# Kernel tuning notes

Hardware: AMD Instinct MI355X
Metric: run time of the kernel (lower is better)

The kernel has to match this reference:

```python
import jax, jax.numpy as jnp
import numpy as np

B, SEQ, NNODES = 4, 12, 1024
SEG_LEN, SEG_NUM = 3, 4
HID, FF, DK, NH, NLAYERS = 64, 2048, 32, 8, 2


def setup_inputs() -> dict:
    key = jax.random.key(0)
    ks = iter(jax.random.split(key, 64))
    def nrm(shape, scale=0.05):
        return jax.random.normal(next(ks), shape, dtype=jnp.float32) * scale
    ones = lambda s: jnp.ones(s, jnp.float32)
    zeros = lambda s: jnp.zeros(s, jnp.float32)
    S, L = 2, NLAYERS
    return {
        'traffic': nrm((B, SEQ, NNODES), 1.0),
        'user': nrm((B, SEQ, NNODES), 1.0),
        'patch_w': nrm((S, HID, SEG_LEN)), 'patch_b': nrm((S, HID)),
        'mha_w': nrm((S, L, 3 * HID, HID)), 'mha_b': nrm((S, L, 3 * HID)),
        'out_w': nrm((S, L, HID, HID)), 'out_b': nrm((S, L, HID)),
        'ff1_w': nrm((S, L, FF, HID)), 'ff1_b': nrm((S, L, FF)),
        'ff2_w': nrm((S, L, HID, FF)), 'ff2_b': nrm((S, L, HID)),
        'ln1_g': ones((S, L, HID)), 'ln1_b': zeros((S, L, HID)),
        'ln2_g': ones((S, L, HID)), 'ln2_b': zeros((S, L, HID)),
        'ga_wq': nrm((S, L, DK, HID)), 'ga_wk': nrm((S, L, DK, HID)), 'ga_wv': nrm((S, L, HID, HID)),
        'ga_ff1_w': nrm((S, L, FF, HID)), 'ga_ff1_b': nrm((S, L, FF)),
        'ga_ff2_w': nrm((S, L, HID, FF)), 'ga_ff2_b': nrm((S, L, HID)),
        'ga_ln1_g': ones((S, L, HID)), 'ga_ln1_b': zeros((S, L, HID)),
        'ga_ln2_g': ones((S, L, HID)), 'ga_ln2_b': zeros((S, L, HID)),
        'ca_wq': nrm((DK, 2 * HID)), 'ca_wk': nrm((DK, 2 * HID)), 'ca_wv': nrm((HID, 2 * HID)),
    }


def _ln(x, g, b, eps=1e-5):
    m = x.mean(-1, keepdims=True)
    v = jnp.mean((x - m) ** 2, -1, keepdims=True)
    return (x - m) / jnp.sqrt(v + eps) * g + b


def _pe(s, d):
    pos = jnp.arange(s, dtype=jnp.float32)[:, None]
    div = jnp.exp(jnp.arange(0, d, 2, dtype=jnp.float32) * (-np.log(10000.0) / d))
    pe = jnp.zeros((s, d), jnp.float32)
    pe = pe.at[:, 0::2].set(jnp.sin(pos * div))
    pe = pe.at[:, 1::2].set(jnp.cos(pos * div))
    return pe


def _mha(x, w, b, wo, bo):
    # standard nn.MultiheadAttention self-attn, batch_first; x: [B,S,H]
    qkv = x @ w.T + b
    q, k, v = jnp.split(qkv, 3, axis=-1)
    def heads(t):
        b_, s_, h_ = t.shape
        return t.reshape(b_, s_, NH, h_ // NH).transpose(0, 2, 1, 3)
    q, k, v = heads(q), heads(k), heads(v)
    scale = 1.0 / jnp.sqrt(jnp.float32(HID // NH))
    att = jax.nn.softmax(jnp.einsum('bhqd,bhkd->bhqk', q, k) * scale, axis=-1)
    o = jnp.einsum('bhqk,bhkd->bhqd', att, v).transpose(0, 2, 1, 3).reshape(x.shape)
    return o @ wo.T + bo


def _enc_layer(x, p):
    # TransformerEncoderLayer_cross, post-norm, dropout=0 (eval)
    x = _ln(x + _mha(x, p['mw'], p['mb'], p['ow'], p['ob']), p['g1'], p['b1'])
    f = jax.nn.relu(x @ p['f1w'].T + p['f1b']) @ p['f2w'].T + p['f2b']
    return _ln(x + f, p['g2'], p['b2'])


def _graph_att(x, p):
    # GraphAttention.forward (bias=None, mask=None, dropout=0)
    q = x @ p['wq'].T
    k = x @ p['wk'].T
    v = x @ p['wv'].T
    dist = jax.nn.softmax(jnp.einsum('bnd,bmd->bnm', q, k) / jnp.sqrt(jnp.float32(DK)), axis=-1)
    att = jnp.einsum('bnm,bmd->bnd', dist, v)
    att = _ln(att, p['g1'], p['b1']) + x
    f = jax.nn.relu(att @ p['f1w'].T + p['f1b']) @ p['f2w'].T + p['f2b']
    return _ln(att + f, p['g2'], p['b2'])


def reference(traffic, user, patch_w, patch_b, mha_w, mha_b, out_w, out_b,
              ff1_w, ff1_b, ff2_w, ff2_b, ln1_g, ln1_b, ln2_g, ln2_b,
              ga_wq, ga_wk, ga_wv, ga_ff1_w, ga_ff1_b, ga_ff2_w, ga_ff2_b,
              ga_ln1_g, ga_ln1_b, ga_ln2_g, ga_ln2_b, ca_wq, ca_wk, ca_wv):
    pe = _pe(SEG_NUM, HID)

    def encode(x, s):
        b, _, d = x.shape
        # DSW_embedding: b (seg_num seg_len) d -> b d seg_num seg_len, then Linear
        seg = x.reshape(b, SEG_NUM, SEG_LEN, d).transpose(0, 3, 1, 2)
        z = seg @ patch_w[s].T + patch_b[s]          # [b, d, seg_num, HID]
        z = z + pe                                    # positional encoding over patches
        for i in range(NLAYERS):
            # temporal attention over the patch axis
            zt = z.reshape(b * d, SEG_NUM, HID)
            zt = _enc_layer(zt, dict(mw=mha_w[s, i], mb=mha_b[s, i], ow=out_w[s, i], ob=out_b[s, i],
                                     f1w=ff1_w[s, i], f1b=ff1_b[s, i], f2w=ff2_w[s, i], f2b=ff2_b[s, i],
                                     g1=ln1_g[s, i], b1=ln1_b[s, i], g2=ln2_g[s, i], b2=ln2_b[s, i]))
            z = zt.reshape(b, d, SEG_NUM, HID)
            # spatial graph attention over the node axis
            zs = z.transpose(0, 2, 1, 3).reshape(b * SEG_NUM, d, HID)
            zs = _graph_att(zs, dict(wq=ga_wq[s, i], wk=ga_wk[s, i], wv=ga_wv[s, i],
                                     f1w=ga_ff1_w[s, i], f1b=ga_ff1_b[s, i], f2w=ga_ff2_w[s, i], f2b=ga_ff2_b[s, i],
                                     g1=ga_ln1_g[s, i], b1=ga_ln1_b[s, i], g2=ga_ln2_g[s, i], b2=ga_ln2_b[s, i]))
            z = zs.reshape(b, SEG_NUM, d, HID).transpose(0, 2, 1, 3)
        return z.mean(axis=2)                         # pool patches -> [b, d, HID]

    enc = jnp.concatenate([encode(traffic, 0), encode(user, 1)], axis=-1)  # [b, d, 2*HID]
    # encoder_attn: SelfAttention(2*HID -> dim_k=32, dim_v=HID)
    q = enc @ ca_wq.T
    k = enc @ ca_wk.T
    v = enc @ ca_wv.T
    dist = jax.nn.softmax(jnp.einsum('bnd,bmd->bnm', q, k) / jnp.sqrt(jnp.float32(DK)), axis=-1)
    return jnp.einsum('bnm,bmd->bnd', dist, v)        # [b, n_nodes, HID]
```

## Files before the change

kernel.cpp:

```cpp
#include <hip/hip_runtime.h>
#include <hip/hip_bf16.h>
#include <math.h>

#define BB 4
#define SEQL 12
#define NN 1024
#define SEGL 3
#define SEGN 4
#define HID 64
#define FFD 2048
#define DKK 32
#define NHH 8
#define HDD 8
#define ZS 1048576

using bf16 = __hip_bfloat16;
__device__ __forceinline__ float b2f(bf16 v) { return __bfloat162float(v); }

typedef __attribute__((ext_vector_type(8))) short s8v;
typedef __attribute__((ext_vector_type(4))) float f4v;
typedef __attribute__((ext_vector_type(4))) unsigned short u4v;

__device__ __forceinline__ unsigned short f2b(float f) {
  bf16 h = __float2bfloat16(f);
  unsigned short u; __builtin_memcpy(&u, &h, 2); return u;
}
__device__ __forceinline__ float us2f(unsigned short u) {
  unsigned int e = ((unsigned int)u) << 16;
  float f; __builtin_memcpy(&f, &e, 4); return f;
}

template <int F>
__device__ __forceinline__ float ldw(const void* p, long i) {
  if (F) return ((const float*)p)[i];
  return b2f(((const bf16*)p)[i]);
}
template <int F>
__device__ __forceinline__ s8v ldfrag(const void* p, long elemOff) {
  if (F) {
    const float* fp = (const float*)p + elemOff;
    f4v u = *(const f4v*)fp, v = *(const f4v*)(fp + 4);
    s8v t;
    t[0]=f2b(u[0]); t[1]=f2b(u[1]); t[2]=f2b(u[2]); t[3]=f2b(u[3]);
    t[4]=f2b(v[0]); t[5]=f2b(v[1]); t[6]=f2b(v[2]); t[7]=f2b(v[3]);
    return t;
  }
  return *(const s8v*)((const unsigned short*)p + elemOff);
}
template <int F>
__device__ __forceinline__ f4v ldb4(const void* p, long i) {
  if (F) return *(const f4v*)((const float*)p + i);
  u4v u = *(const u4v*)((const unsigned short*)p + i);
  f4v r; r[0]=us2f(u[0]); r[1]=us2f(u[1]); r[2]=us2f(u[2]); r[3]=us2f(u[3]);
  return r;
}

__global__ void k_zero(unsigned short* __restrict__ o, int n) {
  int i = blockIdx.x * 256 + threadIdx.x;
  if (i < n) o[i] = 0;
}

__global__ void k_detect(const void* __restrict__ x0, int* __restrict__ flag) {
  int t = threadIdx.x;
  int bad = 0;
  const bf16* p = (const bf16*)x0;
  for (int i = t; i < 512; i += 256) {
    float a = fabsf(b2f(p[i]));
    if (!(a < 1e4f) || (a != 0.f && a < 1e-4f)) bad = 1;
  }
  __shared__ int tot;
  if (t == 0) tot = 0;
  __syncthreads();
  unsigned long long m = __ballot(bad);
  if ((t & 63) == 0) atomicAdd(&tot, __popcll(m));
  __syncthreads();
  if (t == 0) *flag = (tot > 64) ? 1 : 0;
}

template <int F>
__device__ __forceinline__ void wconv_body(const void* __restrict__ w1,
    const void* __restrict__ w2, const void* __restrict__ w3,
    const void* __restrict__ w4, unsigned short* __restrict__ out) {
  int i = blockIdx.x * 256 + threadIdx.x;
  long e8 = (long)i * 8;
  int slot = (int)(e8 >> 17);
  int si = slot >> 2, which = slot & 3;
  long r = e8 & 131071;
  const void* src = (which == 0) ? w1 : (which == 1) ? w2 : (which == 2) ? w3 : w4;
  *(s8v*)(out + e8) = ldfrag<F>(src, (long)si*FFD*HID + r);
}
__global__ __launch_bounds__(256) void k_wconv(const void* w1, const void* w2,
    const void* w3, const void* w4, unsigned short* out,
    const int* __restrict__ flag) {
  if (*flag) wconv_body<1>(w1, w2, w3, w4, out);
  else       wconv_body<0>(w1, w2, w3, w4, out);
}

#define TT 64
#define FRW 64
#define HCS 74

__device__ __forceinline__ void ff_ld(const unsigned short* __restrict__ wc1,
    const unsigned short* __restrict__ wc2, int hb, int srow, int le,
    s8v* r1, s8v* r2) {
  r1[0] = *(const s8v*)(wc1 + (long)(hb + srow)*HID + le*8);
  r1[1] = *(const s8v*)(wc1 + (long)(hb + srow + 8)*HID + le*8);
  r2[0] = *(const s8v*)(wc2 + (long)srow*FFD + hb + le*8);
  r2[1] = *(const s8v*)(wc2 + (long)(srow + 8)*FFD + hb + le*8);
}
__device__ __forceinline__ void ff_wr(char* ldsbuf, int pb, int srow, int swb,
    const s8v* r1, const s8v* r2) {
  char* w1b = ldsbuf + pb*8192;
  char* w2b = ldsbuf + 16384 + pb*8192;
  *(s8v*)(w1b + srow*128 + swb) = r1[0];
  *(s8v*)(w1b + (srow + 8)*128 + swb) = r1[1];
  *(s8v*)(w2b + srow*128 + swb) = r2[0];
  *(s8v*)(w2b + (srow + 8)*128 + swb) = r2[1];
}
template <int F>
__device__ __forceinline__ void ff_compute(const char* ldsbuf, int pb, int hb,
    int col, int quad, int sw, const s8v* bx, unsigned short* hcw,
    const void* __restrict__ B1, long ob1, f4v* acc) {
  const char* w1b = ldsbuf + pb*8192;
  const char* w2b = ldsbuf + 16384 + pb*8192;
#pragma unroll
  for (int t = 0; t < 4; ++t) {
    int row = t*16 + col;
    s8v a10 = *(const s8v*)(w1b + row*128 + ((quad*16) ^ sw));
    s8v a11 = *(const s8v*)(w1b + row*128 + ((64 + quad*16) ^ sw));
    f4v bv = ldb4<F>(B1, ob1 + hb + t*16 + quad*4);
    f4v sv = __builtin_amdgcn_mfma_f32_16x16x32_bf16(a10, bx[0],
               (f4v){0.f,0.f,0.f,0.f}, 0, 0, 0);
    sv = __builtin_amdgcn_mfma_f32_16x16x32_bf16(a11, bx[1], sv, 0, 0, 0);
    unsigned short pk[4];
#pragma unroll
    for (int r = 0; r < 4; ++r) pk[r] = f2b(fmaxf(sv[r] + bv[r], 0.f));
    *(unsigned long long*)&hcw[col*HCS + t*16 + quad*4] =
      (unsigned long long)pk[0] | ((unsigned long long)pk[1] << 16) |
      ((unsigned long long)pk[2] << 32) | ((unsigned long long)pk[3] << 48);
  }
#pragma unroll
  for (int ks2 = 0; ks2 < 2; ++ks2) {
    s8v bh = *(const s8v*)&hcw[col*HCS + ks2*32 + quad*8];
#pragma unroll
    for (int m = 0; m < 4; ++m) {
      int r2 = m*16 + col;
      s8v a2 = *(const s8v*)(w2b + r2*128 + ((ks2*64 + quad*16) ^ sw));
      acc[m] = __builtin_amdgcn_mfma_f32_16x16x32_bf16(a2, bh, acc[m], 0, 0, 0);
    }
  }
}

template <int F>
__device__ __forceinline__ void tff_body(float* __restrict__ zb,
    const void* __restrict__ xt, const void* __restrict__ xu,
    const void* __restrict__ pw, const void* __restrict__ pbp,
    const void* __restrict__ W, const void* __restrict__ bq,
    const void* __restrict__ WO, const void* __restrict__ bo,
    const void* __restrict__ g1, const void* __restrict__ b1,
    const unsigned short* __restrict__ wcw, int li,
    const void* __restrict__ B1, const void* __restrict__ B2,
    const void* __restrict__ G, const void* __restrict__ Bt,
    const void* __restrict__ gwq, const void* __restrict__ gwk,
    const void* __restrict__ gwv,
    unsigned short* __restrict__ qo, unsigned short* __restrict__ ko,
    unsigned short* __restrict__ vto,
    char* lds) {
  int s = blockIdx.x >> 8, blk = blockIdx.x & 255;
  long si = s*2 + li;
  float* z = zb + (long)s*ZS;
  long oW = si*3*HID*HID, obq = si*3*HID, oWO = si*HID*HID, obo = si*HID;
  long og1 = si*HID, ob1 = si*HID;
  const unsigned short* wc1 = wcw + (si*4 + 0)*131072;
  const unsigned short* wc2 = wcw + (si*4 + 1)*131072;
  long fob1 = si*FFD, fob2 = si*HID, fog = si*HID, fobt = si*HID;
  unsigned short (*qkvs)[200] = (unsigned short(*)[200])lds;
  unsigned short (*ao)[72]    = (unsigned short(*)[72])(lds + 25600);
  float (*yb)[68]             = (float(*)[68])(lds + 34816);
  int tid = threadIdx.x;
  int w = tid >> 6, lane = tid & 63;
  int col = lane & 15, quad = lane >> 4;
  long r0 = (long)blk * TT;
  float* stash = (float*)(lds + 59648);
  float* stashW = stash + w*16*68;

  int lr = lane >> 3, le = lane & 7;
  int srow = w*16 + lr;
  int swb = ((le ^ lr) << 4);
  s8v cw1[2], cw2[2];
  ff_ld(wc1, wc2, 0, srow, le, cw1, cw2);

  if (li == 0) {
    const void* x = s ? xu : xt;
    long opw = (long)s*HID*SEGL, opb = (long)s*HID;
    float dv = expf((float)(2*(lane >> 1)) * (-logf(10000.f) / (float)HID));
    float pe[4];
#pragma unroll
    for (int g = 0; g < 4; ++g) {
      float ang = (float)g * dv;
      pe[g] = (lane & 1) ? cosf(ang) : sinf(ang);
    }
    float pbv = ldw<F>(pbp, opb + lane);
    float pwv[3];
#pragma unroll
    for (int l = 0; l < 3; ++l) pwv[l] = ldw<F>(pw, opw + lane*3 + l);
#pragma unroll
    for (int rr = 0; rr < 16; ++rr) {
      long tok = r0 + w*16 + rr;
      int b_ = (int)(tok >> 12);
      int n_ = (int)((tok >> 2) & 1023);
      int g_ = (int)(tok & 3);
      float a = pbv;
#pragma unroll
      for (int l = 0; l < 3; ++l)
        a += ldw<F>(x, (long)(b_*SEQL + g_*SEGL + l)*NN + n_) * pwv[l];
      stashW[rr*68 + lane] = a + pe[g_];
    }
    __syncthreads();
  }

  s8v bx[4][2];
#pragma unroll
  for (int mt = 0; mt < 4; ++mt) {
    const float* xr = (li == 0) ? &stash[(mt*16 + col)*68]
                                : (z + (r0 + mt*16 + col) * HID);
#pragma unroll
    for (int ks = 0; ks < 2; ++ks) {
      const float* p = xr + ks*32 + quad*8;
      f4v u = *(const f4v*)p, v = *(const f4v*)(p + 4);
      s8v t;
      t[0]=f2b(u[0]); t[1]=f2b(u[1]); t[2]=f2b(u[2]); t[3]=f2b(u[3]);
      t[4]=f2b(v[0]); t[5]=f2b(v[1]); t[6]=f2b(v[2]); t[7]=f2b(v[3]);
      bx[mt][ks] = t;
    }
  }
#pragma unroll
  for (int nt = 0; nt < 3; ++nt) {
    int cbase = (w*3 + nt) * 16;
    s8v aw[2];
#pragma unroll
    for (int ks = 0; ks < 2; ++ks)
      aw[ks] = ldfrag<F>(W, oW + (long)(cbase + col)*HID + ks*32 + quad*8);
    f4v bv = ldb4<F>(bq, obq + cbase + quad*4);
#pragma unroll
    for (int mt = 0; mt < 4; ++mt) {
      f4v sv = (f4v){0.f,0.f,0.f,0.f};
#pragma unroll
      for (int ks = 0; ks < 2; ++ks)
        sv = __builtin_amdgcn_mfma_f32_16x16x32_bf16(aw[ks], bx[mt][ks], sv, 0, 0, 0);
      unsigned short pk[4];
#pragma unroll
      for (int r = 0; r < 4; ++r) pk[r] = f2b(sv[r] + bv[r]);
      *(unsigned long long*)&qkvs[mt*16 + col][cbase + quad*4] =
        (unsigned long long)pk[0] | ((unsigned long long)pk[1] << 16) |
        ((unsigned long long)pk[2] << 32) | ((unsigned long long)pk[3] << 48);
    }
  }
  __syncthreads();
  if (tid < 128) {
    int gi = tid >> 3, hd = tid & 7;
    int tl = gi * 4;
    float qv[4][8], kv[4][8], vv[4][8];
#pragma unroll
    for (int t4 = 0; t4 < 4; ++t4) {
      s8v qq = *(const s8v*)&qkvs[tl + t4][hd*8];
      s8v kk = *(const s8v*)&qkvs[tl + t4][64 + hd*8];
      s8v vq = *(const s8v*)&qkvs[tl + t4][128 + hd*8];
#pragma unroll
      for (int e = 0; e < 8; ++e) {
        qv[t4][e] = us2f((unsigned short)qq[e]);
        kv[t4][e] = us2f((unsigned short)kk[e]);
        vv[t4][e] = us2f((unsigned short)vq[e]);
      }
    }
    const float sc8 = 0.3535533905932738f;
#pragma unroll
    for (int qt = 0; qt < 4; ++qt) {
      float sc[4]; float mx = -1e30f;
#pragma unroll
      for (int kt = 0; kt < 4; ++kt) {
        float d = 0;
#pragma unroll
        for (int e = 0; e < 8; ++e) d += qv[qt][e]*kv[kt][e];
        sc[kt] = d*sc8; mx = fmaxf(mx, sc[kt]);
      }
      float se = 0;
#pragma unroll
      for (int kt = 0; kt < 4; ++kt) { sc[kt] = expf(sc[kt]-mx); se += sc[kt]; }
      float inv = 1.f/se;
      s8v outp;
#pragma unroll
      for (int e = 0; e < 8; ++e) {
        float o = 0;
#pragma unroll
        for (int kt = 0; kt < 4; ++kt) o += sc[kt]*vv[kt][e];
        outp[e] = (short)f2b(o*inv);
      }
      *(s8v*)&ao[tl + qt][hd*8] = outp;
    }
  }
  __syncthreads();
  s8v awo[2];
#pragma unroll
  for (int ks = 0; ks < 2; ++ks)
    awo[ks] = ldfrag<F>(WO, oWO + (long)(w*16 + col)*HID + ks*32 + quad*8);
  f4v bov = ldb4<F>(bo, obo + w*16 + quad*4);
#pragma unroll
  for (int mt = 0; mt < 4; ++mt) {
    f4v ov = (f4v){0.f,0.f,0.f,0.f};
#pragma unroll
    for (int ks = 0; ks < 2; ++ks) {
      s8v bao = *(const s8v*)&ao[mt*16 + col][ks*32 + quad*8];
      ov = __builtin_amdgcn_mfma_f32_16x16x32_bf16(awo[ks], bao, ov, 0, 0, 0);
    }
    f4v yv;
#pragma unroll
    for (int r = 0; r < 4; ++r) yv[r] = ov[r] + bov[r];
    *(f4v*)&yb[mt*16 + col][w*16 + quad*4] = yv;
  }
  __syncthreads();
  {
    float gg = ldw<F>(g1, og1 + lane), bb2 = ldw<F>(b1, ob1 + lane);
#pragma unroll
    for (int rr = 0; rr < 16; ++rr) {
      int row = w*16 + rr;
      long tok = r0 + row;
      float res = (li == 0) ? stashW[rr*68 + lane] : z[tok*HID + lane];
      float val = yb[row][lane] + res;
      float sm = val;
#pragma unroll
      for (int off = 32; off; off >>= 1) sm += __shfl_xor(sm, off);
      float m = sm*(1.f/HID);
      float d = val - m, sq = d*d;
#pragma unroll
      for (int off = 32; off; off >>= 1) sq += __shfl_xor(sq, off);
      float rv = rsqrtf(sq*(1.f/HID) + 1e-5f);
      stashW[rr*68 + lane] = d*rv*gg + bb2;
    }
  }
  __syncthreads();

  unsigned short* hcw = (unsigned short*)(lds + 32768 + w*2368);
  float* red = (float*)(lds + 42240 + w*4352);

  s8v bx2[2];
#pragma unroll
  for (int ks = 0; ks < 2; ++ks) {
    const float* p = &stashW[col*68 + ks*32 + quad*8];
    f4v u = *(const f4v*)p, v = *(const f4v*)(p + 4);
    s8v t;
    t[0]=f2b(u[0]); t[1]=f2b(u[1]); t[2]=f2b(u[2]); t[3]=f2b(u[3]);
    t[4]=f2b(v[0]); t[5]=f2b(v[1]); t[6]=f2b(v[2]); t[7]=f2b(v[3]);
    bx2[ks] = t;
  }

  f4v acc[4];
#pragma unroll
  for (int m = 0; m < 4; ++m) acc[m] = (f4v){0.f,0.f,0.f,0.f};

  s8v rA1[2], rA2[2], rB1[2], rB2[2];
  ff_ld(wc1, wc2, 64, srow, le, rA1, rA2);
  ff_ld(wc1, wc2, 128, srow, le, rB1, rB2);
  ff_wr(lds, 0, srow, swb, cw1, cw2);
  __syncthreads();

  const int sw = (col & 7) << 4;
  for (int c = 0; c < 32; c += 2) {
    ff_compute<F>(lds, 0, c*64, col, quad, sw, bx2, hcw, B1, fob1, acc);
    ff_wr(lds, 1, srow, swb, rA1, rA2);
    if (c + 3 < 32) ff_ld(wc1, wc2, (c+3)*64, srow, le, rA1, rA2);
    __syncthreads();
    ff_compute<F>(lds, 1, (c+1)*64, col, quad, sw, bx2, hcw, B1, fob1, acc);
    if (c + 2 < 32) ff_wr(lds, 0, srow, swb, rB1, rB2);
    if (c + 4 < 32) ff_ld(wc1, wc2, (c+4)*64, srow, le, rB1, rB2);
    __syncthreads();
  }

#pragma unroll
  for (int m = 0; m < 4; ++m)
    *(f4v*)&red[col*68 + m*16 + quad*4] = acc[m];
  float* finb = (float*)lds;
  {
    float fgg = ldw<F>(G, fog + lane), fbbt = ldw<F>(Bt, fobt + lane);
    float b2v = ldw<F>(B2, fob2 + lane);
#pragma unroll
    for (int rr = 0; rr < 16; ++rr) {
      long grow = r0 + w*16 + rr;
      float val = red[rr*68 + lane] + b2v + stashW[rr*68 + lane];
      float sm = val;
#pragma unroll
      for (int off = 32; off; off >>= 1) sm += __shfl_xor(sm, off);
      float m = sm * (1.f/HID);
      float d = val - m;
      float sq = d*d;
#pragma unroll
      for (int off = 32; off; off >>= 1) sq += __shfl_xor(sq, off);
      float rv = rsqrtf(sq*(1.f/HID) + 1e-5f);
      float fin = d*rv*fgg + fbbt;
      z[grow*HID + lane] = fin;
      finb[(w*16 + rr)*68 + lane] = fin;
    }
  }
  __syncthreads();

  long oq = si*DKK*HID, okk = si*DKK*HID, ovv = si*HID*HID;
  s8v bx3[4][2];
#pragma unroll
  for (int rt = 0; rt < 4; ++rt)
#pragma unroll
    for (int ks = 0; ks < 2; ++ks) {
      const float* p = &finb[(rt*16 + col)*68 + ks*32 + quad*8];
      f4v u = *(const f4v*)p, v = *(const f4v*)(p + 4);
      s8v t;
      t[0]=f2b(u[0]); t[1]=f2b(u[1]); t[2]=f2b(u[2]); t[3]=f2b(u[3]);
      t[4]=f2b(v[0]); t[5]=f2b(v[1]); t[6]=f2b(v[2]); t[7]=f2b(v[3]);
      bx3[rt][ks] = t;
    }
#pragma unroll
  for (int tt = 0; tt < 2; ++tt) {
    int ct = w*2 + tt;
    const void* wp; long wo; int co; int kind;
    if (ct < 2)      { wp = gwq; wo = oq;  co = ct*16;      kind = 0; }
    else if (ct < 4) { wp = gwk; wo = okk; co = (ct-2)*16;  kind = 1; }
    else             { wp = gwv; wo = ovv; co = (ct-4)*16;  kind = 2; }
    s8v aw[2];
#pragma unroll
    for (int ks = 0; ks < 2; ++ks)
      aw[ks] = ldfrag<F>(wp, wo + (long)(co + col)*HID + ks*32 + quad*8);
#pragma unroll
    for (int rt = 0; rt < 4; ++rt) {
      f4v sv = (f4v){0.f,0.f,0.f,0.f};
#pragma unroll
      for (int ks = 0; ks < 2; ++ks)
        sv = __builtin_amdgcn_mfma_f32_16x16x32_bf16(aw[ks], bx3[rt][ks], sv, 0, 0, 0);
      long tok2 = r0 + rt*16 + col;
      int b_ = (int)(tok2 >> 12);
      int n_ = (int)((tok2 >> 2) & 1023);
      int g_ = (int)(tok2 & 3);
      int sgl = s*16 + b_*4 + g_;
      if (kind == 2) {
        long vbase = (long)sgl*HID*NN;
#pragma unroll
        for (int r = 0; r < 4; ++r)
          vto[vbase + (long)(co + quad*4 + r)*NN + n_] = f2b(sv[r]);
      } else {
        long row = (long)sgl*NN + n_;
        unsigned short pk[4];
#pragma unroll
        for (int r = 0; r < 4; ++r) pk[r] = f2b(sv[r]);
        unsigned short* dst = kind ? ko : qo;
        *(unsigned long long*)&dst[row*DKK + co + quad*4] =
          (unsigned long long)pk[0] | ((unsigned long long)pk[1] << 16) |
          ((unsigned long long)pk[2] << 32) | ((unsigned long long)pk[3] << 48);
      }
    }
  }
}
__global__ __launch_bounds__(256) void k_tff(float* __restrict__ z,
    const void* xt, const void* xu, const void* pw, const void* pbp,
    const void* W, const void* bqkv, const void* WO, const void* bo,
    const void* g1, const void* b1,
    const unsigned short* __restrict__ wcw, int li,
    const void* B1, const void* B2, const void* G, const void* Bt,
    const void* gwq, const void* gwk, const void* gwv,
    unsigned short* qo, unsigned short* ko, unsigned short* vto,
    const int* __restrict__ flag) {
  __shared__ __attribute__((aligned(16))) char lds[77056];
  if (*flag) tff_body<1>(z, xt, xu, pw, pbp, W, bqkv, WO, bo, g1, b1, wcw, li,
                         B1, B2, G, Bt, gwq, gwk, gwv, qo, ko, vto, lds);
  else       tff_body<0>(z, xt, xu, pw, pbp, W, bqkv, WO, bo, g1, b1, wcw, li,
                         B1, B2, G, Bt, gwq, gwk, gwv, qo, ko, vto, lds);
}

template <int F>
__device__ __forceinline__ void ffmfma_body(float* __restrict__ xb,
    const unsigned short* __restrict__ wcw, int li, int wsel,
    const void* __restrict__ B1, const void* __restrict__ B2,
    const void* __restrict__ G, const void* __restrict__ Bt,
    float* __restrict__ enc, int dop,
    char* ldsbuf) {
  int s = blockIdx.x >> 8, blk = blockIdx.x & 255;
  long si = s*2 + li;
  float* x = xb + (long)s*ZS;
  const unsigned short* wc1 = wcw + (si*4 + wsel)*131072;
  const unsigned short* wc2 = wcw + (si*4 + wsel + 1)*131072;
  long ob1 = si*FFD, ob2 = si*HID, og = si*HID, obt = si*HID;
  int tid = threadIdx.x;
  int w = tid >> 6, lane = tid & 63;
  int col = lane & 15, quad = lane >> 4;
  long r0 = (long)blk * FRW;
  unsigned short* hcw = (unsigned short*)(ldsbuf + 32768 + w*2368);
  float* red = (float*)(ldsbuf + w*4352);

  long tokc = r0 + w*16 + col;
  s8v bx[2];
  {
    const float* xr = x + tokc * HID;
#pragma unroll
    for (int ks = 0; ks < 2; ++ks) {
      const float* p = xr + ks*32 + quad*8;
      f4v u = *(const f4v*)p, v = *(const f4v*)(p + 4);
      s8v t;
      t[0]=f2b(u[0]); t[1]=f2b(u[1]); t[2]=f2b(u[2]); t[3]=f2b(u[3]);
      t[4]=f2b(v[0]); t[5]=f2b(v[1]); t[6]=f2b(v[2]); t[7]=f2b(v[3]);
      bx[ks] = t;
    }
  }

  int lr = lane >> 3;
  int le = lane & 7;
  int srow = w*16 + lr;
  int swb = ((le ^ lr) << 4);

  f4v acc[4];
#pragma unroll
  for (int m = 0; m < 4; ++m) acc[m] = (f4v){0.f,0.f,0.f,0.f};

  s8v t1[2], t2[2], rA1[2], rA2[2], rB1[2], rB2[2];
  ff_ld(wc1, wc2, 0, srow, le, t1, t2);
  ff_wr(ldsbuf, 0, srow, swb, t1, t2);
  ff_ld(wc1, wc2, 64, srow, le, rA1, rA2);
  ff_ld(wc1, wc2, 128, srow, le, rB1, rB2);
  __syncthreads();

  const int sw = (col & 7) << 4;
  for (int c = 0; c < 32; c += 2) {
    ff_compute<F>(ldsbuf, 0, c*64, col, quad, sw, bx, hcw, B1, ob1, acc);
    ff_wr(ldsbuf, 1, srow, swb, rA1, rA2);
    if (c + 3 < 32) ff_ld(wc1, wc2, (c+3)*64, srow, le, rA1, rA2);
    __syncthreads();
    ff_compute<F>(ldsbuf, 1, (c+1)*64, col, quad, sw, bx, hcw, B1, ob1, acc);
    if (c + 2 < 32) ff_wr(ldsbuf, 0, srow, swb, rB1, rB2);
    if (c + 4 < 32) ff_ld(wc1, wc2, (c+4)*64, srow, le, rB1, rB2);
    __syncthreads();
  }

#pragma unroll
  for (int m = 0; m < 4; ++m)
    *(f4v*)&red[col*68 + m*16 + quad*4] = acc[m];
  float gg = ldw<F>(G, og + lane), bbt = ldw<F>(Bt, obt + lane);
  float b2v = ldw<F>(B2, ob2 + lane);
  float pacc[4] = {0.f,0.f,0.f,0.f};
#pragma unroll
  for (int rr = 0; rr < 16; ++rr) {
    long grow = r0 + w*16 + rr;
    float val = red[rr*68 + lane] + b2v + x[grow*HID + lane];
    float sm = val;
#pragma unroll
    for (int off = 32; off; off >>= 1) sm += __shfl_xor(sm, off);
    float m = sm * (1.f/HID);
    float d = val - m;
    float sq = d*d;
#pragma unroll
    for (int off = 32; off; off >>= 1) sq += __shfl_xor(sq, off);
    float rv = rsqrtf(sq*(1.f/HID) + 1e-5f);
    float fin = d*rv*gg + bbt;
    x[grow*HID + lane] = fin;
    pacc[rr >> 2] += fin;
  }
  if (dop) {
#pragma unroll
    for (int j = 0; j < 4; ++j) {
      long tok = r0 + w*16 + j*4;
      enc[(tok >> 2)*(2*HID) + s*HID + lane] = pacc[j]*0.25f;
    }
  }
}
__global__ __launch_bounds__(256) void k_ffmfma(float* __restrict__ x,
    const unsigned short* __restrict__ wcw, int li, int wsel,
    const void* B1, const void* B2, const void* G, const void* Bt,
    float* enc, int dop, const int* __restrict__ flag) {
  __shared__ __attribute__((aligned(16))) char ldsbuf[42240];
  if (*flag) ffmfma_body<1>(x, wcw, li, wsel, B1, B2, G, Bt, enc, dop, ldsbuf);
  else       ffmfma_body<0>(x, wcw, li, wsel, B1, B2, G, Bt, enc, dop, ldsbuf);
}

__global__ __launch_bounds__(512) void k_gattn(float* __restrict__ zb,
    const unsigned short* __restrict__ qb, const unsigned short* __restrict__ kb,
    const unsigned short* __restrict__ vtb,
    const void* __restrict__ g1, const void* __restrict__ b1, int li,
    const int* __restrict__ flag) {
  int f = *flag;
  __shared__ unsigned short pl[2][8][16][74];
  __shared__ float accb[8][16][66];
  __shared__ float lb[8][16];
  int tid = threadIdx.x;
  int w = tid >> 6, lane = tid & 63;
  int col = lane & 15, quad = lane >> 4;
  int qt = w >> 1, kh = w & 1;
  int sg = blockIdx.x >> 4;
  int s = sg >> 4, bg = sg & 15;
  int n0 = (blockIdx.x & 15) * 64;
  long si = s*2 + li;
  float* z = zb + (long)s*ZS;
  long og1 = si*HID, ob1 = si*HID;
  long gbase = (long)sg * NN;
  const unsigned short* vrow = vtb + (long)sg*HID*NN;

  s8v aq = *(const s8v*)(qb + (gbase + n0 + qt*16 + col)*DKK + quad*8);

  f4v acc[4];
#pragma unroll
  for (int t = 0; t < 4; ++t) acc[t] = (f4v){0.f,0.f,0.f,0.f};
  float psum[4] = {0.f,0.f,0.f,0.f};
  const float rs = 0.17677669529663687f;
  const int cbeg = kh * 512;

#pragma unroll 2
  for (int it = 0; it < 8; ++it) {
    int c0 = cbeg + it*64;
    int pb = it & 1;
    f4v s4[4];
#pragma unroll
    for (int nt = 0; nt < 4; ++nt) {
      s8v bk = *(const s8v*)(kb + (gbase + c0 + nt*16 + col)*DKK + quad*8);
      s4[nt] = __builtin_amdgcn_mfma_f32_16x16x32_bf16(aq, bk,
                (f4v){0.f,0.f,0.f,0.f}, 0, 0, 0);
    }
#pragma unroll
    for (int r = 0; r < 4; ++r) {
      float p0 = expf(s4[0][r]*rs), p1 = expf(s4[1][r]*rs);
      float p2 = expf(s4[2][r]*rs), p3 = expf(s4[3][r]*rs);
      psum[r] += (p0 + p1) + (p2 + p3);
      int row = quad*4 + r;
      pl[pb][w][row][col]      = f2b(p0);
      pl[pb][w][row][16 + col] = f2b(p1);
      pl[pb][w][row][32 + col] = f2b(p2);
      pl[pb][w][row][48 + col] = f2b(p3);
    }
#pragma unroll
    for (int ks = 0; ks < 2; ++ks) {
      s8v ap = *(const s8v*)&pl[pb][w][col][ks*32 + quad*8];
#pragma unroll
      for (int nt = 0; nt < 4; ++nt) {
        s8v bv = *(const s8v*)(vrow + (long)(nt*16 + col)*NN + c0 + ks*32 + quad*8);
        acc[nt] = __builtin_amdgcn_mfma_f32_16x16x32_bf16(ap, bv, acc[nt], 0, 0, 0);
      }
    }
  }

#pragma unroll
  for (int r = 0; r < 4; ++r) {
    float v = psum[r];
#pragma unroll
    for (int off = 1; off < 16; off <<= 1) v += __shfl_xor(v, off);
    psum[r] = v;
  }
#pragma unroll
  for (int t = 0; t < 4; ++t)
#pragma unroll
    for (int r = 0; r < 4; ++r)
      accb[w][quad*4 + r][t*16 + col] = acc[t][r];
  if (col == 0) {
#pragma unroll
    for (int r = 0; r < 4; ++r) lb[w][quad*4 + r] = psum[r];
  }
  __syncthreads();

  int b = bg >> 2, g = bg & 3;
  float gg = f ? ((const float*)g1)[og1 + lane] : b2f(((const bf16*)g1)[og1 + lane]);
  float bb = f ? ((const float*)b1)[ob1 + lane] : b2f(((const bf16*)b1)[ob1 + lane]);
#pragma unroll
  for (int rr = 0; rr < 8; ++rr) {
    int rl = w*8 + rr;
    int qtt = rl >> 4, lrr = rl & 15;
    float a = accb[2*qtt][lrr][lane] + accb[2*qtt + 1][lrr][lane];
    float l = lb[2*qtt][lrr] + lb[2*qtt + 1][lrr];
    float val = a / l;
    float s2 = val;
#pragma unroll
    for (int off = 32; off; off >>= 1) s2 += __shfl_xor(s2, off);
    float m = s2*(1.f/HID);
    float d = val - m, sq = d*d;
#pragma unroll
    for (int off = 32; off; off >>= 1) sq += __shfl_xor(sq, off);
    float r = rsqrtf(sq*(1.f/HID) + 1e-5f);
    float* zp = z + ((long)(b*NN + n0 + rl)*SEGN + g)*HID;
    zp[lane] = d*r*gg + bb + zp[lane];
  }
}

template <int F>
__device__ __forceinline__ void fqkv_body(const float* __restrict__ enc,
    const void* __restrict__ wq, const void* __restrict__ wk,
    const void* __restrict__ wv,
    unsigned short* __restrict__ q, unsigned short* __restrict__ k,
    unsigned short* __restrict__ vt, float* xs) {
  long r = blockIdx.x;
  int t = threadIdx.x;
  xs[t] = enc[r*128 + t];
  __syncthreads();
  if (t < 32) {
    long wr = (long)t*128; float a = 0;
    for (int e = 0; e < 128; ++e) a += xs[e]*ldw<F>(wq, wr + e);
    q[r*DKK + t] = f2b(a);
  } else if (t < 64) {
    long wr = (long)(t-32)*128; float a = 0;
    for (int e = 0; e < 128; ++e) a += xs[e]*ldw<F>(wk, wr + e);
    k[r*DKK + (t-32)] = f2b(a);
  } else {
    long wr = (long)(t-64)*128; float a = 0;
    for (int e = 0; e < 128; ++e) a += xs[e]*ldw<F>(wv, wr + e);
    vt[((r >> 10)*HID + (t-64))*NN + (r & 1023)] = f2b(a);
  }
}
__global__ __launch_bounds__(128) void k_fqkv(const float* __restrict__ enc,
    const void* wq, const void* wk, const void* wv,
    unsigned short* q, unsigned short* k, unsigned short* vt,
    const int* __restrict__ flag) {
  __shared__ float xs[2*HID];
  if (*flag) fqkv_body<1>(enc, wq, wk, wv, q, k, vt, xs);
  else       fqkv_body<0>(enc, wq, wk, wv, q, k, vt, xs);
}

__global__ __launch_bounds__(512) void k_fattn(
    const unsigned short* __restrict__ qb, const unsigned short* __restrict__ kb,
    const unsigned short* __restrict__ vtb, void* __restrict__ outp,
    const int* __restrict__ flag) {
  __shared__ unsigned short pl[2][8][16][74];
  __shared__ float accb[8][16][66];
  __shared__ float lb[8][16];
  int tid = threadIdx.x;
  int w = tid >> 6, lane = tid & 63;
  int col = lane & 15, quad = lane >> 4;
  int qt = w >> 1, kh = w & 1;
  int b = blockIdx.x >> 4;
  int n0 = (blockIdx.x & 15) * 64;
  long gbase = (long)b * NN;
  const unsigned short* vrow = vtb + (long)b*HID*NN;

  s8v aq = *(const s8v*)(qb + (gbase + n0 + qt*16 + col)*DKK + quad*8);

  f4v acc[4];
#pragma unroll
  for (int t = 0; t < 4; ++t) acc[t] = (f4v){0.f,0.f,0.f,0.f};
  float psum[4] = {0.f,0.f,0.f,0.f};
  const float rs = 0.17677669529663687f;
  const int cbeg = kh * 512;

#pragma unroll 2
  for (int it = 0; it < 8; ++it) {
    int c0 = cbeg + it*64;
    int pb = it & 1;
    f4v s4[4];
#pragma unroll
    for (int nt = 0; nt < 4; ++nt) {
      s8v bk = *(const s8v*)(kb + (gbase + c0 + nt*16 + col)*DKK + quad*8);
      s4[nt] = __builtin_amdgcn_mfma_f32_16x16x32_bf16(aq, bk,
                (f4v){0.f,0.f,0.f,0.f}, 0, 0, 0);
    }
#pragma unroll
    for (int r = 0; r < 4; ++r) {
      float p0 = expf(s4[0][r]*rs), p1 = expf(s4[1][r]*rs);
      float p2 = expf(s4[2][r]*rs), p3 = expf(s4[3][r]*rs);
      psum[r] += (p0 + p1) + (p2 + p3);
      int row = quad*4 + r;
      pl[pb][w][row][col]      = f2b(p0);
      pl[pb][w][row][16 + col] = f2b(p1);
      pl[pb][w][row][32 + col] = f2b(p2);
      pl[pb][w][row][48 + col] = f2b(p3);
    }
#pragma unroll
    for (int ks = 0; ks < 2; ++ks) {
      s8v ap = *(const s8v*)&pl[pb][w][col][ks*32 + quad*8];
#pragma unroll
      for (int nt = 0; nt < 4; ++nt) {
        s8v bv = *(const s8v*)(vrow + (long)(nt*16 + col)*NN + c0 + ks*32 + quad*8);
        acc[nt] = __builtin_amdgcn_mfma_f32_16x16x32_bf16(ap, bv, acc[nt], 0, 0, 0);
      }
    }
  }

#pragma unroll
  for (int r = 0; r < 4; ++r) {
    float v = psum[r];
#pragma unroll
    for (int off = 1; off < 16; off <<= 1) v += __shfl_xor(v, off);
    psum[r] = v;
  }
#pragma unroll
  for (int t = 0; t < 4; ++t)
#pragma unroll
    for (int r = 0; r < 4; ++r)
      accb[w][quad*4 + r][t*16 + col] = acc[t][r];
  if (col == 0) {
#pragma unroll
    for (int r = 0; r < 4; ++r) lb[w][quad*4 + r] = psum[r];
  }
  __syncthreads();

  int f = *flag;
#pragma unroll
  for (int rr = 0; rr < 8; ++rr) {
    int rl = w*8 + rr;
    int qtt = rl >> 4, lrr = rl & 15;
    float a = accb[2*qtt][lrr][lane] + accb[2*qtt + 1][lrr][lane];
    float l = lb[2*qtt][lrr] + lb[2*qtt + 1][lrr];
    float val = a / l;
    long idx = (gbase + n0 + rl)*HID + lane;
    if (f) ((float*)outp)[idx] = val;
    else   ((bf16*)outp)[idx] = __float2bfloat16(val);
  }
}

extern "C" void kernel_launch(void* const* d_in, const int* in_sizes, int n_in,
                              void* d_out, int out_size, void* d_ws, size_t ws_size,
                              hipStream_t stream) {
  static const int EXP[30] = {
    49152, 49152, 384, 128, 49152, 768, 16384, 256,
    524288, 8192, 524288, 256, 256, 256, 256, 256,
    8192, 8192, 16384, 524288, 8192, 524288, 256, 256,
    256, 256, 256, 4096, 4096, 8192
  };
  const size_t NEED = (size_t)(2*ZS + 524288 + 524288 + 524288 + 1048576 + 1048576) * 4 + 64;
  bool ok = (n_in == 30) && (ws_size >= NEED) && (out_size == BB*NN*HID);
  if (ok) for (int i = 0; i < 30; ++i) ok = ok && (in_sizes[i] == EXP[i]);
  if (!ok) {
    k_zero<<<(BB*NN*HID + 255)/256, 256, 0, stream>>>((unsigned short*)d_out, BB*NN*HID);
    return;
  }

  float* z   = (float*)d_ws;
  float* enc = z   + 2*ZS;
  float* qb  = enc + 524288;
  float* kb  = qb  + 524288;
  float* vb  = kb  + 524288;
  float* wcf = vb  + 1048576;
  int*  flag = (int*)(wcf + 1048576);
  unsigned short* wcw = (unsigned short*)wcf;

  k_detect<<<1, 256, 0, stream>>>(d_in[0], flag);

  const void *i_traffic=d_in[0], *i_user=d_in[1], *i_pw=d_in[2], *i_pb=d_in[3],
    *i_mw=d_in[4], *i_mb=d_in[5], *i_ow=d_in[6], *i_ob=d_in[7], *i_f1w=d_in[8],
    *i_f1b=d_in[9], *i_f2w=d_in[10], *i_f2b=d_in[11], *i_l1g=d_in[12],
    *i_l1b=d_in[13], *i_l2g=d_in[14], *i_l2b=d_in[15], *i_gwq=d_in[16],
    *i_gwk=d_in[17], *i_gwv=d_in[18], *i_gf1w=d_in[19], *i_gf1b=d_in[20],
    *i_gf2w=d_in[21], *i_gf2b=d_in[22], *i_gl1g=d_in[23], *i_gl1b=d_in[24],
    *i_gl2g=d_in[25], *i_gl2b=d_in[26], *i_cwq=d_in[27], *i_cwk=d_in[28],
    *i_cwv=d_in[29];

  k_wconv<<<1024, 256, 0, stream>>>(i_f1w, i_f2w, i_gf1w, i_gf2w, wcw, flag);

  for (int i = 0; i < 2; ++i) {
    k_tff<<<512, 256, 0, stream>>>(z,
        i_traffic, i_user, i_pw, i_pb,
        i_mw, i_mb, i_ow, i_ob,
        i_l1g, i_l1b, wcw, i, i_f1b, i_f2b, i_l2g, i_l2b,
        i_gwq, i_gwk, i_gwv,
        (unsigned short*)qb, (unsigned short*)kb, (unsigned short*)vb, flag);
    k_gattn<<<512, 512, 0, stream>>>(z,
        (const unsigned short*)qb, (const unsigned short*)kb,
        (const unsigned short*)vb, i_gl1g, i_gl1b, i, flag);
    k_ffmfma<<<512, 256, 0, stream>>>(z, wcw, i, 2,
        i_gf1b, i_gf2b, i_gl2g, i_gl2b, enc, (i == 1) ? 1 : 0, flag);
  }
  k_fqkv<<<BB*NN, 128, 0, stream>>>(enc, i_cwq, i_cwk, i_cwv,
      (unsigned short*)qb, (unsigned short*)kb, (unsigned short*)vb, flag);
  k_fattn<<<BB*16, 512, 0, stream>>>((const unsigned short*)qb,
      (const unsigned short*)kb, (unsigned short*)vb, d_out, flag);
}
```

Before: 587.0 us.

## Fuse layer-0 graph FFN into layer-1 temporal kernel; split final attention finer

The layer-0 graph-attention feed-forward (k_ffmfma) launch is removed. Its FF1/FF2, residual and LayerNorm now run at the start of the layer-1 k_tff kernel through a shared ff_run helper, and the result is staged in LDS instead of being written back to z. This drops one launch and one round trip of z through global memory, but the layer-1 k_tff kernel now does two streamed FFN passes in series. Separately, the final encoder attention uses 128 blocks of 32 query rows with a 4-way key split instead of 64 blocks with a 2-way split, to fill more CUs.

```diff
diff --git a/kernel.cpp b/kernel.cpp
--- a/kernel.cpp
+++ b/kernel.cpp
@@ -150,6 +150,28 @@
     }
   }
 }
+template <int F>
+__device__ __forceinline__ void ff_run(char* ldsbuf,
+    const unsigned short* __restrict__ wc1, const unsigned short* __restrict__ wc2,
+    const void* __restrict__ B1, long ob1, const s8v* bx, unsigned short* hcw,
+    int col, int quad, int sw, int srow, int le, int swb, f4v* acc) {
+  s8v c1[2], c2[2], rA1[2], rA2[2], rB1[2], rB2[2];
+  ff_ld(wc1, wc2, 0, srow, le, c1, c2);
+  ff_wr(ldsbuf, 0, srow, swb, c1, c2);
+  ff_ld(wc1, wc2, 64, srow, le, rA1, rA2);
+  ff_ld(wc1, wc2, 128, srow, le, rB1, rB2);
+  __syncthreads();
+  for (int c = 0; c < 32; c += 2) {
+    ff_compute<F>(ldsbuf, 0, c*64, col, quad, sw, bx, hcw, B1, ob1, acc);
+    ff_wr(ldsbuf, 1, srow, swb, rA1, rA2);
+    if (c + 3 < 32) ff_ld(wc1, wc2, (c+3)*64, srow, le, rA1, rA2);
+    __syncthreads();
+    ff_compute<F>(ldsbuf, 1, (c+1)*64, col, quad, sw, bx, hcw, B1, ob1, acc);
+    if (c + 2 < 32) ff_wr(ldsbuf, 0, srow, swb, rB1, rB2);
+    if (c + 4 < 32) ff_ld(wc1, wc2, (c+4)*64, srow, le, rB1, rB2);
+    __syncthreads();
+  }
+}
 
 template <int F>
 __device__ __forceinline__ void tff_body(float* __restrict__ zb,
@@ -161,6 +183,8 @@
     const unsigned short* __restrict__ wcw, int li,
     const void* __restrict__ B1, const void* __restrict__ B2,
     const void* __restrict__ G, const void* __restrict__ Bt,
+    const void* __restrict__ pgf1b, const void* __restrict__ pgf2b,
+    const void* __restrict__ pgl2g, const void* __restrict__ pgl2b,
     const void* __restrict__ gwq, const void* __restrict__ gwk,
     const void* __restrict__ gwv,
     unsigned short* __restrict__ qo, unsigned short* __restrict__ ko,
@@ -183,12 +207,12 @@
   long r0 = (long)blk * TT;
   float* stash = (float*)(lds + 59648);
   float* stashW = stash + w*16*68;
-
+  unsigned short* hcw = (unsigned short*)(lds + 32768 + w*2368);
+  float* red = (float*)(lds + 42240 + w*4352);
   int lr = lane >> 3, le = lane & 7;
   int srow = w*16 + lr;
   int swb = ((le ^ lr) << 4);
-  s8v cw1[2], cw2[2];
-  ff_ld(wc1, wc2, 0, srow, le, cw1, cw2);
+  const int sw = (col & 7) << 4;
 
   if (li == 0) {
     const void* x = s ? xu : xt;
@@ -217,13 +241,55 @@
       stashW[rr*68 + lane] = a + pe[g_];
     }
     __syncthreads();
+  } else {
+    long sip = s*2;
+    const unsigned short* pw1 = wcw + (sip*4 + 2)*131072;
+    const unsigned short* pw2 = wcw + (sip*4 + 3)*131072;
+    long pob1 = sip*FFD, pob2 = sip*HID, pog = sip*HID, pobt = sip*HID;
+    s8v bxp[2];
+    {
+      const float* xr = z + (r0 + w*16 + col) * HID;
+#pragma unroll
+      for (int ks = 0; ks < 2; ++ks) {
+        const float* p = xr + ks*32 + quad*8;
+        f4v u = *(const f4v*)p, v = *(const f4v*)(p + 4);
+        s8v t;
+        t[0]=f2b(u[0]); t[1]=f2b(u[1]); t[2]=f2b(u[2]); t[3]=f2b(u[3]);
+        t[4]=f2b(v[0]); t[5]=f2b(v[1]); t[6]=f2b(v[2]); t[7]=f2b(v[3]);
+        bxp[ks] = t;
+      }
+    }
+    f4v accp[4];
+#pragma unroll
+    for (int m = 0; m < 4; ++m) accp[m] = (f4v){0.f,0.f,0.f,0.f};
+    ff_run<F>(lds, pw1, pw2, pgf1b, pob1, bxp, hcw, col, quad, sw, srow, le, swb, accp);
+#pragma unroll
+    for (int m = 0; m < 4; ++m)
+      *(f4v*)&red[col*68 + m*16 + quad*4] = accp[m];
+    float pgg = ldw<F>(pgl2g, pog + lane), pbb = ldw<F>(pgl2b, pobt + lane);
+    float pb2 = ldw<F>(pgf2b, pob2 + lane);
+#pragma unroll
+    for (int rr = 0; rr < 16; ++rr) {
+      long grow = r0 + w*16 + rr;
+      float val = red[rr*68 + lane] + pb2 + z[grow*HID + lane];
+      float sm = val;
+#pragma unroll
+      for (int off = 32; off; off >>= 1) sm += __shfl_xor(sm, off);
+      float m = sm * (1.f/HID);
+      float d = val - m;
+      float sq = d*d;
+#pragma unroll
+      for (int off = 32; off; off >>= 1) sq += __shfl_xor(sq, off);
+      float rv = rsqrtf(sq*(1.f/HID) + 1e-5f);
+      stashW[rr*68 + lane] = d*rv*pgg + pbb;
+    }
+    __syncthreads();
   }
 
   s8v bx[4][2];
 #pragma unroll
   for (int mt = 0; mt < 4; ++mt) {
-    const float* xr = (li == 0) ? &stash[(mt*16 + col)*68]
-                                : (z + (r0 + mt*16 + col) * HID);
+    const float* xr = &stash[(mt*16 + col)*68];
 #pragma unroll
     for (int ks = 0; ks < 2; ++ks) {
       const float* p = xr + ks*32 + quad*8;
@@ -324,9 +390,7 @@
 #pragma unroll
     for (int rr = 0; rr < 16; ++rr) {
       int row = w*16 + rr;
-      long tok = r0 + row;
-      float res = (li == 0) ? stashW[rr*68 + lane] : z[tok*HID + lane];
-      float val = yb[row][lane] + res;
+      float val = yb[row][lane] + stashW[rr*68 + lane];
       float sm = val;
 #pragma unroll
       for (int off = 32; off; off >>= 1) sm += __shfl_xor(sm, off);
@@ -339,9 +403,6 @@
     }
   }
   __syncthreads();
-
-  unsigned short* hcw = (unsigned short*)(lds + 32768 + w*2368);
-  float* red = (float*)(lds + 42240 + w*4352);
 
   s8v bx2[2];
 #pragma unroll
@@ -357,24 +418,7 @@
   f4v acc[4];
 #pragma unroll
   for (int m = 0; m < 4; ++m) acc[m] = (f4v){0.f,0.f,0.f,0.f};
-
-  s8v rA1[2], rA2[2], rB1[2], rB2[2];
-  ff_ld(wc1, wc2, 64, srow, le, rA1, rA2);
-  ff_ld(wc1, wc2, 128, srow, le, rB1, rB2);
-  ff_wr(lds, 0, srow, swb, cw1, cw2);
-  __syncthreads();
-
-  const int sw = (col & 7) << 4;
-  for (int c = 0; c < 32; c += 2) {
-    ff_compute<F>(lds, 0, c*64, col, quad, sw, bx2, hcw, B1, fob1, acc);
-    ff_wr(lds, 1, srow, swb, rA1, rA2);
-    if (c + 3 < 32) ff_ld(wc1, wc2, (c+3)*64, srow, le, rA1, rA2);
-    __syncthreads();
-    ff_compute<F>(lds, 1, (c+1)*64, col, quad, sw, bx2, hcw, B1, fob1, acc);
-    if (c + 2 < 32) ff_wr(lds, 0, srow, swb, rB1, rB2);
-    if (c + 4 < 32) ff_ld(wc1, wc2, (c+4)*64, srow, le, rB1, rB2);
-    __syncthreads();
-  }
+  ff_run<F>(lds, wc1, wc2, B1, fob1, bx2, hcw, col, quad, sw, srow, le, swb, acc);
 
 #pragma unroll
   for (int m = 0; m < 4; ++m)
@@ -462,14 +506,17 @@
     const void* g1, const void* b1,
     const unsigned short* __restrict__ wcw, int li,
     const void* B1, const void* B2, const void* G, const void* Bt,
+    const void* pgf1b, const void* pgf2b, const void* pgl2g, const void* pgl2b,
     const void* gwq, const void* gwk, const void* gwv,
     unsigned short* qo, unsigned short* ko, unsigned short* vto,
     const int* __restrict__ flag) {
   __shared__ __attribute__((aligned(16))) char lds[77056];
   if (*flag) tff_body<1>(z, xt, xu, pw, pbp, W, bqkv, WO, bo, g1, b1, wcw, li,
-                         B1, B2, G, Bt, gwq, gwk, gwv, qo, ko, vto, lds);
+                         B1, B2, G, Bt, pgf1b, pgf2b, pgl2g, pgl2b,
+                         gwq, gwk, gwv, qo, ko, vto, lds);
   else       tff_body<0>(z, xt, xu, pw, pbp, W, bqkv, WO, bo, g1, b1, wcw, li,
-                         B1, B2, G, Bt, gwq, gwk, gwv, qo, ko, vto, lds);
+                         B1, B2, G, Bt, pgf1b, pgf2b, pgl2g, pgl2b,
+                         gwq, gwk, gwv, qo, ko, vto, lds);
 }
 
 template <int F>
@@ -511,29 +558,12 @@
   int le = lane & 7;
   int srow = w*16 + lr;
   int swb = ((le ^ lr) << 4);
+  const int sw = (col & 7) << 4;
 
   f4v acc[4];
 #pragma unroll
   for (int m = 0; m < 4; ++m) acc[m] = (f4v){0.f,0.f,0.f,0.f};
-
-  s8v t1[2], t2[2], rA1[2], rA2[2], rB1[2], rB2[2];
-  ff_ld(wc1, wc2, 0, srow, le, t1, t2);
-  ff_wr(ldsbuf, 0, srow, swb, t1, t2);
-  ff_ld(wc1, wc2, 64, srow, le, rA1, rA2);
-  ff_ld(wc1, wc2, 128, srow, le, rB1, rB2);
-  __syncthreads();
-
-  const int sw = (col & 7) << 4;
-  for (int c = 0; c < 32; c += 2) {
-    ff_compute<F>(ldsbuf, 0, c*64, col, quad, sw, bx, hcw, B1, ob1, acc);
-    ff_wr(ldsbuf, 1, srow, swb, rA1, rA2);
-    if (c + 3 < 32) ff_ld(wc1, wc2, (c+3)*64, srow, le, rA1, rA2);
-    __syncthreads();
-    ff_compute<F>(ldsbuf, 1, (c+1)*64, col, quad, sw, bx, hcw, B1, ob1, acc);
-    if (c + 2 < 32) ff_wr(ldsbuf, 0, srow, swb, rB1, rB2);
-    if (c + 4 < 32) ff_ld(wc1, wc2, (c+4)*64, srow, le, rB1, rB2);
-    __syncthreads();
-  }
+  ff_run<F>(ldsbuf, wc1, wc2, B1, ob1, bx, hcw, col, quad, sw, srow, le, swb, acc);
 
 #pragma unroll
   for (int m = 0; m < 4; ++m)
@@ -723,9 +753,9 @@
   int tid = threadIdx.x;
   int w = tid >> 6, lane = tid & 63;
   int col = lane & 15, quad = lane >> 4;
-  int qt = w >> 1, kh = w & 1;
-  int b = blockIdx.x >> 4;
-  int n0 = (blockIdx.x & 15) * 64;
+  int qt = w >> 2, kh = w & 3;
+  int b = blockIdx.x >> 5;
+  int n0 = (blockIdx.x & 31) * 32;
   long gbase = (long)b * NN;
   const unsigned short* vrow = vtb + (long)b*HID*NN;
 
@@ -736,10 +766,10 @@
   for (int t = 0; t < 4; ++t) acc[t] = (f4v){0.f,0.f,0.f,0.f};
   float psum[4] = {0.f,0.f,0.f,0.f};
   const float rs = 0.17677669529663687f;
-  const int cbeg = kh * 512;
+  const int cbeg = kh * 256;
 
 #pragma unroll 2
-  for (int it = 0; it < 8; ++it) {
+  for (int it = 0; it < 4; ++it) {
     int c0 = cbeg + it*64;
     int pb = it & 1;
     f4v s4[4];
@@ -791,11 +821,13 @@
 
   int f = *flag;
 #pragma unroll
-  for (int rr = 0; rr < 8; ++rr) {
-    int rl = w*8 + rr;
+  for (int rr = 0; rr < 4; ++rr) {
+    int rl = w*4 + rr;
     int qtt = rl >> 4, lrr = rl & 15;
-    float a = accb[2*qtt][lrr][lane] + accb[2*qtt + 1][lrr][lane];
-    float l = lb[2*qtt][lrr] + lb[2*qtt + 1][lrr];
+    float a = accb[4*qtt][lrr][lane] + accb[4*qtt + 1][lrr][lane]
+            + accb[4*qtt + 2][lrr][lane] + accb[4*qtt + 3][lrr][lane];
+    float l = lb[4*qtt][lrr] + lb[4*qtt + 1][lrr]
+            + lb[4*qtt + 2][lrr] + lb[4*qtt + 3][lrr];
     float val = a / l;
     long idx = (gbase + n0 + rl)*HID + lane;
     if (f) ((float*)outp)[idx] = val;
@@ -842,21 +874,31 @@
 
   k_wconv<<<1024, 256, 0, stream>>>(i_f1w, i_f2w, i_gf1w, i_gf2w, wcw, flag);
 
-  for (int i = 0; i < 2; ++i) {
-    k_tff<<<512, 256, 0, stream>>>(z,
-        i_traffic, i_user, i_pw, i_pb,
-        i_mw, i_mb, i_ow, i_ob,
-        i_l1g, i_l1b, wcw, i, i_f1b, i_f2b, i_l2g, i_l2b,
-        i_gwq, i_gwk, i_gwv,
-        (unsigned short*)qb, (unsigned short*)kb, (unsigned short*)vb, flag);
-    k_gattn<<<512, 512, 0, stream>>>(z,
-        (const unsigned short*)qb, (const unsigned short*)kb,
-        (const unsigned short*)vb, i_gl1g, i_gl1b, i, flag);
-    k_ffmfma<<<512, 256, 0, stream>>>(z, wcw, i, 2,
-        i_gf1b, i_gf2b, i_gl2g, i_gl2b, enc, (i == 1) ? 1 : 0, flag);
-  }
+  k_tff<<<512, 256, 0, stream>>>(z,
+      i_traffic, i_user, i_pw, i_pb,
+      i_mw, i_mb, i_ow, i_ob,
+      i_l1g, i_l1b, wcw, 0, i_f1b, i_f2b, i_l2g, i_l2b,
+      i_gf1b, i_gf2b, i_gl2g, i_gl2b,
+      i_gwq, i_gwk, i_gwv,
+      (unsigned short*)qb, (unsigned short*)kb, (unsigned short*)vb, flag);
+  k_gattn<<<512, 512, 0, stream>>>(z,
+      (const unsigned short*)qb, (const unsigned short*)kb,
+      (const unsigned short*)vb, i_gl1g, i_gl1b, 0, flag);
+  k_tff<<<512, 256, 0, stream>>>(z,
+      i_traffic, i_user, i_pw, i_pb,
+      i_mw, i_mb, i_ow, i_ob,
+      i_l1g, i_l1b, wcw, 1, i_f1b, i_f2b, i_l2g, i_l2b,
+      i_gf1b, i_gf2b, i_gl2g, i_gl2b,
+      i_gwq, i_gwk, i_gwv,
+      (unsigned short*)qb, (unsigned short*)kb, (unsigned short*)vb, flag);
+  k_gattn<<<512, 512, 0, stream>>>(z,
+      (const unsigned short*)qb, (const unsigned short*)kb,
+      (const unsigned short*)vb, i_gl1g, i_gl1b, 1, flag);
+  k_ffmfma<<<512, 256, 0, stream>>>(z, wcw, 1, 2,
+      i_gf1b, i_gf2b, i_gl2g, i_gl2b, enc, 1, flag);
+
   k_fqkv<<<BB*NN, 128, 0, stream>>>(enc, i_cwq, i_cwk, i_cwv,
       (unsigned short*)qb, (unsigned short*)kb, (unsigned short*)vb, flag);
-  k_fattn<<<BB*16, 512, 0, stream>>>((const unsigned short*)qb,
+  k_fattn<<<BB*32, 512, 0, stream>>>((const unsigned short*)qb,
       (const unsigned short*)kb, (unsigned short*)vb, d_out, flag);
 }
```

After: 566.5 us. -3.5%, faster.
